# Kernel optimization log

Hardware: AMD Instinct MI355X
Metric: run time of the kernel (lower is better)

## Reference

```python
import jax, jax.numpy as jnp
import numpy as np

N_SRC, N_DST, K = 50000, 10000, 32
IN_F, OUT_F, H, L = 256, 128, 8, 10


def setup_inputs() -> dict:
    key = jax.random.key(0)
    ks = jax.random.split(key, 12)
    s = 0.05
    return {
        "feat": jax.random.normal(ks[0], (N_SRC, IN_F), jnp.float32),
        "labels": jax.random.uniform(ks[1], (N_SRC, L), jnp.float32),
        "labels_ori": jax.random.uniform(ks[2], (N_SRC, L), jnp.float32),
        "label_rela": jax.random.uniform(ks[3], (L, L), jnp.float32),
        "W_neigh": jax.random.normal(ks[4], (IN_F, OUT_F), jnp.float32) * s,
        "b_neigh": jnp.zeros((OUT_F,), jnp.float32),
        "W_self": jax.random.normal(ks[5], (IN_F, OUT_F), jnp.float32) * s,
        "b_self": jnp.zeros((OUT_F,), jnp.float32),
        "W_attn": jax.random.normal(ks[6], (2 * OUT_F, OUT_F * H), jnp.float32) * s,
        "b_attn": jnp.zeros((OUT_F * H,), jnp.float32),
        "feat_attn_W": jax.random.normal(ks[7], (1, H, OUT_F), jnp.float32) * s,
        "eps": jnp.full((1,), 0.5, jnp.float32),
        "out_bias": jnp.zeros((OUT_F,), jnp.float32),
        "nbr_idx": jax.random.randint(ks[8], (N_DST, K), 0, N_SRC, jnp.int32),
    }


def reference(feat, labels, labels_ori, label_rela, W_neigh, b_neigh, W_self,
              b_self, W_attn, b_attn, feat_attn_W, eps, out_bias, nbr_idx):
    n_dst = nbr_idx.shape[0]
    # lin_before_mp is True (in_feats > out_feats): fc_neigh applied to src feats
    h_src = feat @ W_neigh + b_neigh                      # (N_SRC, OUT_F)
    feat_dst = feat[:n_dst]
    cent_l = labels[:n_dst]                                # dst predicted labels
    cent_f = h_src[:n_dst]                                 # dst 'f' field
    # mailbox gather: fixed-fanout neighbors
    h = h_src[nbr_idx]                                     # (N, K, OUT_F)
    l_pred = labels[nbr_idx]                               # (N, K, L)
    # label similarity: sum(outer(l_pred_j, cent_l_i) * R)
    label_sim = jnp.einsum('nka,ab,nb->nk', l_pred, label_rela, cent_l)
    # feature attention score
    h_act = jax.nn.leaky_relu(h, negative_slope=0.1)
    cent_rep = jnp.broadcast_to(cent_f[:, None, :], h_act.shape)
    x = jnp.concatenate([h_act, cent_rep], axis=-1)        # (N, K, 2*OUT_F)
    t = (x @ W_attn + b_attn).reshape(n_dst, K, H, OUT_F)
    feat_sim = jnp.einsum('nkhd,hd->nk', t, feat_attn_W[0])
    # merge (torch.tensor(...) in the original detaches this from the graph)
    merge = jax.lax.stop_gradient(label_sim * eps[0] + feat_sim * (1.0 - eps[0]))
    att = jax.nn.softmax(merge, axis=1)                    # (N, K)
    neigh = (h * att[:, :, None]).mean(axis=1)             # (N, OUT_F)
    rst = (feat_dst @ W_self + b_self + neigh) * 0.5 + out_bias
    return rst, cent_l, labels_ori[:n_dst]
```

## Files before the change

kernel.cpp:

```cpp
#include <hip/hip_runtime.h>
#include <hip/hip_bf16.h>

#define N_SRC 50000
#define N_DST 10000
#define KNBR  32
#define IN_F  256
#define OUT_F 128
#define LDIM  10
#define ATTN_OUT 1024
#define NB_BIG  782
#define NB_SELF 157

using f32x4 = __attribute__((ext_vector_type(4))) float;
using s16x8 = __attribute__((ext_vector_type(8))) short;

#define OUT_CENT (N_DST*OUT_F)
#define OUT_LORI (N_DST*OUT_F + N_DST*LDIM)

#define WS_WCOMB 0
#define WS_BN    128
#define WS_BS    (128 + 16384)
#define WS_HSRC  (128 + 32768)
#define WS_SELF0 (128 + 32768 + (N_SRC*OUT_F/2))

__device__ __forceinline__ ushort f2bf(float x) {
  __hip_bfloat16 h = __float2bfloat16(x);
  return *reinterpret_cast<ushort*>(&h);
}

__global__ __launch_bounds__(256) void prep_kernel(
    const float* __restrict__ W_attn, const float* __restrict__ fW,
    const float* __restrict__ W_neigh, const float* __restrict__ W_self,
    float* __restrict__ w_comb, ushort* __restrict__ Bn, ushort* __restrict__ Bs) {
  const int b = blockIdx.x;
  const int t = threadIdx.x;
  if (b < 128) {
    __shared__ float red[256];
    float s = 0.f;
#pragma unroll
    for (int i = 0; i < 4; ++i) {
      int o = t + i * 256;
      s += W_attn[(size_t)b * ATTN_OUT + o] * fW[o];
    }
    red[t] = s;
    __syncthreads();
    for (int st = 128; st > 0; st >>= 1) {
      if (t < st) red[t] += red[t + st];
      __syncthreads();
    }
    if (t == 0) w_comb[b] = red[0];
  } else if (b < 256) {
    int k = 2 * (b - 128) + (t >> 7);
    int n = t & 127;
    float x = W_neigh[(size_t)k * OUT_F + n];
    Bn[(k >> 3) * 1024 + n * 8 + (k & 7)] = f2bf(x);
  } else {
    int k = 2 * (b - 256) + (t >> 7);
    int n = t & 127;
    float x = W_self[(size_t)k * OUT_F + n];
    Bs[(k >> 3) * 1024 + n * 8 + (k & 7)] = f2bf(x);
  }
}

template<bool OUT_BF16>
__device__ __forceinline__ void gemm_body(
    const float* __restrict__ A, const ushort* __restrict__ Bp,
    const float* __restrict__ bias, void* __restrict__ C, int M, int m0) {
  const int t = threadIdx.x;
  const int wv = t >> 6, ln = t & 63;
  const int dg = ln & 15, kg = ln >> 4;
  int r = m0 + wv * 16 + dg;
  r = r < M ? r : M - 1;

  f32x4 araw[16];
  const float* arow = &A[(size_t)r * IN_F];
#pragma unroll
  for (int k0 = 0; k0 < 8; ++k0) {
    const f32x4* ap = (const f32x4*)&arow[k0 * 32 + kg * 8];
    araw[2 * k0]     = ap[0];
    araw[2 * k0 + 1] = ap[1];
  }
  s16x8 afr[8];
#pragma unroll
  for (int k0 = 0; k0 < 8; ++k0) {
    s16x8 f;
    f[0] = (short)f2bf(araw[2*k0][0]); f[1] = (short)f2bf(araw[2*k0][1]);
    f[2] = (short)f2bf(araw[2*k0][2]); f[3] = (short)f2bf(araw[2*k0][3]);
    f[4] = (short)f2bf(araw[2*k0+1][0]); f[5] = (short)f2bf(araw[2*k0+1][1]);
    f[6] = (short)f2bf(araw[2*k0+1][2]); f[7] = (short)f2bf(araw[2*k0+1][3]);
    afr[k0] = f;
  }

  f32x4 acc[8];
#pragma unroll
  for (int ct = 0; ct < 8; ++ct) acc[ct] = (f32x4){0.f, 0.f, 0.f, 0.f};
#pragma unroll
  for (int k0 = 0; k0 < 8; ++k0) {
    const ushort* bb = Bp + (k0 * 4 + kg) * 1024 + dg * 8;
#pragma unroll
    for (int ct = 0; ct < 8; ++ct) {
      s16x8 bfr = *reinterpret_cast<const s16x8*>(bb + ct * 128);
      acc[ct] = __builtin_amdgcn_mfma_f32_16x16x32_bf16(afr[k0], bfr, acc[ct], 0, 0, 0);
    }
  }

#pragma unroll
  for (int ct = 0; ct < 8; ++ct) {
    int col = ct * 16 + dg;
    float bb = bias[col];
#pragma unroll
    for (int e = 0; e < 4; ++e) {
      int rr = m0 + wv * 16 + kg * 4 + e;
      if (rr < M) {
        float v = acc[ct][e] + bb;
        if (OUT_BF16) ((ushort*)C)[(size_t)rr * OUT_F + col] = f2bf(v);
        else          ((float*)C)[(size_t)rr * OUT_F + col] = v;
      }
    }
  }
}

__global__ __launch_bounds__(256) void fused_gemm(
    const float* __restrict__ A,
    const ushort* __restrict__ Bn, const ushort* __restrict__ Bs,
    const float* __restrict__ bias_n, const float* __restrict__ bias_s,
    ushort* __restrict__ hsrc, float* __restrict__ self0) {
  if (blockIdx.x < NB_BIG)
    gemm_body<true>(A, Bn, bias_n, (void*)hsrc, N_SRC, blockIdx.x * 64);
  else
    gemm_body<false>(A, Bs, bias_s, (void*)self0, N_DST, (blockIdx.x - NB_BIG) * 64);
}

__global__ __launch_bounds__(256) void attn_kernel(
    const float* __restrict__ labels, const float* __restrict__ labels_ori,
    const float* __restrict__ label_rela, const int* __restrict__ nbr_idx,
    const ushort* __restrict__ hsrc, const float* __restrict__ self0,
    const float* __restrict__ w_comb, const float* __restrict__ eps_p,
    const float* __restrict__ out_bias, float* __restrict__ out) {
  const int t = threadIdx.x;
  const int wv = t >> 6, ln = t & 63;
  const int n = blockIdx.x * 4 + wv;
  const int dg = ln & 15, kg = ln >> 4;

  const float eps = eps_p[0];
  const float om = 1.f - eps;

  float wcs[8];
  {
    const f32x4* wp = (const f32x4*)&w_comb[dg * 8];
    f32x4 w0 = wp[0], w1 = wp[1];
    wcs[0] = om * w0[0]; wcs[1] = om * w0[1]; wcs[2] = om * w0[2]; wcs[3] = om * w0[3];
    wcs[4] = om * w1[0]; wcs[5] = om * w1[1]; wcs[6] = om * w1[2]; wcs[7] = om * w1[3];
  }
  float va = 0.f;
  if (dg < LDIM) {
#pragma unroll
    for (int b = 0; b < LDIM; ++b)
      va += label_rela[dg * LDIM + b] * labels[(size_t)n * LDIM + b];
    va *= eps;
  }

  const int* irow = nbr_idx + (size_t)n * KNBR;
  float hf[8][8];
  float m[8];
#pragma unroll
  for (int j = 0; j < 8; ++j) {
    int id = irow[kg * 8 + j];
    uint4 hv = *(const uint4*)(hsrc + (size_t)id * OUT_F + dg * 8);
    hf[j][0] = __uint_as_float(hv.x << 16);
    hf[j][1] = __uint_as_float(hv.x & 0xffff0000u);
    hf[j][2] = __uint_as_float(hv.y << 16);
    hf[j][3] = __uint_as_float(hv.y & 0xffff0000u);
    hf[j][4] = __uint_as_float(hv.z << 16);
    hf[j][5] = __uint_as_float(hv.z & 0xffff0000u);
    hf[j][6] = __uint_as_float(hv.w << 16);
    hf[j][7] = __uint_as_float(hv.w & 0xffff0000u);
    float p = 0.f;
#pragma unroll
    for (int e = 0; e < 8; ++e)
      p = fmaf(fmaxf(hf[j][e], 0.1f * hf[j][e]), wcs[e], p);
    if (dg < LDIM) p = fmaf(labels[(size_t)id * LDIM + dg], va, p);
    m[j] = p;
  }
#pragma unroll
  for (int s = 1; s < 16; s <<= 1) {
#pragma unroll
    for (int j = 0; j < 8; ++j) m[j] += __shfl_xor(m[j], s);
  }
  float mx = m[0];
#pragma unroll
  for (int j = 1; j < 8; ++j) mx = fmaxf(mx, m[j]);
  mx = fmaxf(mx, __shfl_xor(mx, 16));
  mx = fmaxf(mx, __shfl_xor(mx, 32));
  float ssum = 0.f;
#pragma unroll
  for (int j = 0; j < 8; ++j) {
    m[j] = __expf(m[j] - mx);
    ssum += m[j];
  }
  ssum += __shfl_xor(ssum, 16);
  ssum += __shfl_xor(ssum, 32);
  const float scale = 1.f / (ssum * (float)KNBR);
  float pn[8];
#pragma unroll
  for (int e = 0; e < 8; ++e) pn[e] = 0.f;
#pragma unroll
  for (int j = 0; j < 8; ++j) {
#pragma unroll
    for (int e = 0; e < 8; ++e) pn[e] = fmaf(m[j], hf[j][e], pn[e]);
  }
#pragma unroll
  for (int e = 0; e < 8; ++e) {
    pn[e] += __shfl_xor(pn[e], 16);
    pn[e] += __shfl_xor(pn[e], 32);
  }
  if (kg == 0) {
    const float* srow = self0 + (size_t)n * OUT_F + dg * 8;
    float* orow = out + (size_t)n * OUT_F + dg * 8;
    f32x4 o0, o1;
#pragma unroll
    for (int e = 0; e < 4; ++e)
      o0[e] = (srow[e] + pn[e] * scale) * 0.5f + out_bias[dg * 8 + e];
#pragma unroll
    for (int e = 0; e < 4; ++e)
      o1[e] = (srow[4 + e] + pn[4 + e] * scale) * 0.5f + out_bias[dg * 8 + 4 + e];
    *(f32x4*)orow = o0;
    *(f32x4*)(orow + 4) = o1;
  }
  if (kg == 1 && dg < LDIM)
    out[OUT_CENT + (size_t)n * LDIM + dg] = labels[(size_t)n * LDIM + dg];
  if (kg == 2 && dg < LDIM)
    out[OUT_LORI + (size_t)n * LDIM + dg] = labels_ori[(size_t)n * LDIM + dg];
}

extern "C" void kernel_launch(void* const* d_in, const int* in_sizes, int n_in,
                              void* d_out, int out_size, void* d_ws, size_t ws_size,
                              hipStream_t stream) {
  const float* feat       = (const float*)d_in[0];
  const float* labels     = (const float*)d_in[1];
  const float* labels_ori = (const float*)d_in[2];
  const float* label_rela = (const float*)d_in[3];
  const float* W_neigh    = (const float*)d_in[4];
  const float* b_neigh    = (const float*)d_in[5];
  const float* W_self     = (const float*)d_in[6];
  const float* b_self     = (const float*)d_in[7];
  const float* W_attn     = (const float*)d_in[8];
  const float* fW         = (const float*)d_in[10];
  const float* eps        = (const float*)d_in[11];
  const float* out_bias   = (const float*)d_in[12];
  const int*   nbr_idx    = (const int*)d_in[13];

  float* wsf = (float*)d_ws;
  float* out = (float*)d_out;

  float*  w_comb = wsf + WS_WCOMB;
  ushort* Bn     = (ushort*)(wsf + WS_BN);
  ushort* Bsf    = (ushort*)(wsf + WS_BS);
  ushort* h_src  = (ushort*)(wsf + WS_HSRC);
  float*  self0  = wsf + WS_SELF0;

  prep_kernel<<<384, 256, 0, stream>>>(W_attn, fW, W_neigh, W_self, w_comb, Bn, Bsf);
  fused_gemm<<<NB_BIG + NB_SELF, 256, 0, stream>>>(feat, Bn, Bsf, b_neigh, b_self, h_src, self0);
  attn_kernel<<<(N_DST / 4), 256, 0, stream>>>(labels, labels_ori, label_rela, nbr_idx,
                                               h_src, self0, w_comb, eps, out_bias, out);
}
```

Before: 65.75 us.

## Precompute per-source feature attention score in GEMM epilogue, gather scalar in attn

The feature-similarity score leaky_relu(h)·w_comb depends only on the source node, so it is now computed once per source row in the GEMM epilogue from the fp32 accumulator and stored in a score array. The attention kernel gathers one scalar per neighbor instead of recomputing the dot product for each of the 32 neighbor occurrences. This removes redundant ALU work there. It also issues all neighbor row loads before use and adds launch_bounds occupancy hints. The cost is a cross-lane reduction in the GEMM epilogue and an extra small gather. The score now uses unrounded fp32 values rather than bf16-rounded ones, which slightly changes numerics.

```diff
diff --git a/kernel.cpp b/kernel.cpp
--- a/kernel.cpp
+++ b/kernel.cpp
@@ -22,6 +22,7 @@
 #define WS_BS    (128 + 16384)
 #define WS_HSRC  (128 + 32768)
 #define WS_SELF0 (128 + 32768 + (N_SRC*OUT_F/2))
+#define WS_SCORE (WS_SELF0 + N_DST*OUT_F)
 
 __device__ __forceinline__ ushort f2bf(float x) {
   __hip_bfloat16 h = __float2bfloat16(x);
@@ -65,30 +66,34 @@
 template<bool OUT_BF16>
 __device__ __forceinline__ void gemm_body(
     const float* __restrict__ A, const ushort* __restrict__ Bp,
-    const float* __restrict__ bias, void* __restrict__ C, int M, int m0) {
+    const float* __restrict__ bias, const float* __restrict__ w_comb,
+    void* __restrict__ C, float* __restrict__ score_f, int M, int m0) {
   const int t = threadIdx.x;
   const int wv = t >> 6, ln = t & 63;
   const int dg = ln & 15, kg = ln >> 4;
   int r = m0 + wv * 16 + dg;
   r = r < M ? r : M - 1;
-
-  f32x4 araw[16];
   const float* arow = &A[(size_t)r * IN_F];
-#pragma unroll
-  for (int k0 = 0; k0 < 8; ++k0) {
-    const f32x4* ap = (const f32x4*)&arow[k0 * 32 + kg * 8];
-    araw[2 * k0]     = ap[0];
-    araw[2 * k0 + 1] = ap[1];
-  }
+
   s16x8 afr[8];
 #pragma unroll
-  for (int k0 = 0; k0 < 8; ++k0) {
-    s16x8 f;
-    f[0] = (short)f2bf(araw[2*k0][0]); f[1] = (short)f2bf(araw[2*k0][1]);
-    f[2] = (short)f2bf(araw[2*k0][2]); f[3] = (short)f2bf(araw[2*k0][3]);
-    f[4] = (short)f2bf(araw[2*k0+1][0]); f[5] = (short)f2bf(araw[2*k0+1][1]);
-    f[6] = (short)f2bf(araw[2*k0+1][2]); f[7] = (short)f2bf(araw[2*k0+1][3]);
-    afr[k0] = f;
+  for (int half = 0; half < 2; ++half) {
+    f32x4 araw[8];
+#pragma unroll
+    for (int k0 = 0; k0 < 4; ++k0) {
+      const f32x4* ap = (const f32x4*)&arow[(half * 4 + k0) * 32 + kg * 8];
+      araw[2 * k0]     = ap[0];
+      araw[2 * k0 + 1] = ap[1];
+    }
+#pragma unroll
+    for (int k0 = 0; k0 < 4; ++k0) {
+      s16x8 f;
+      f[0] = (short)f2bf(araw[2*k0][0]); f[1] = (short)f2bf(araw[2*k0][1]);
+      f[2] = (short)f2bf(araw[2*k0][2]); f[3] = (short)f2bf(araw[2*k0][3]);
+      f[4] = (short)f2bf(araw[2*k0+1][0]); f[5] = (short)f2bf(araw[2*k0+1][1]);
+      f[6] = (short)f2bf(araw[2*k0+1][2]); f[7] = (short)f2bf(araw[2*k0+1][3]);
+      afr[half * 4 + k0] = f;
+    }
   }
 
   f32x4 acc[8];
@@ -104,38 +109,57 @@
     }
   }
 
+  float sc[4] = {0.f, 0.f, 0.f, 0.f};
 #pragma unroll
   for (int ct = 0; ct < 8; ++ct) {
     int col = ct * 16 + dg;
     float bb = bias[col];
+    float wc = OUT_BF16 ? w_comb[col] : 0.f;
 #pragma unroll
     for (int e = 0; e < 4; ++e) {
       int rr = m0 + wv * 16 + kg * 4 + e;
-      if (rr < M) {
-        float v = acc[ct][e] + bb;
-        if (OUT_BF16) ((ushort*)C)[(size_t)rr * OUT_F + col] = f2bf(v);
-        else          ((float*)C)[(size_t)rr * OUT_F + col] = v;
+      float v = acc[ct][e] + bb;
+      if (OUT_BF16) {
+        sc[e] = fmaf(fmaxf(v, 0.1f * v), wc, sc[e]);
+        if (rr < M) ((ushort*)C)[(size_t)rr * OUT_F + col] = f2bf(v);
+      } else {
+        if (rr < M) ((float*)C)[(size_t)rr * OUT_F + col] = v;
       }
     }
   }
-}
-
-__global__ __launch_bounds__(256) void fused_gemm(
+  if (OUT_BF16) {
+#pragma unroll
+    for (int s = 1; s < 16; s <<= 1) {
+#pragma unroll
+      for (int e = 0; e < 4; ++e) sc[e] += __shfl_xor(sc[e], s);
+    }
+    if (dg == 0) {
+#pragma unroll
+      for (int e = 0; e < 4; ++e) {
+        int rr = m0 + wv * 16 + kg * 4 + e;
+        if (rr < M) score_f[rr] = sc[e];
+      }
+    }
+  }
+}
+
+__global__ __launch_bounds__(256, 4) void fused_gemm(
     const float* __restrict__ A,
     const ushort* __restrict__ Bn, const ushort* __restrict__ Bs,
     const float* __restrict__ bias_n, const float* __restrict__ bias_s,
-    ushort* __restrict__ hsrc, float* __restrict__ self0) {
+    const float* __restrict__ w_comb,
+    ushort* __restrict__ hsrc, float* __restrict__ self0, float* __restrict__ score_f) {
   if (blockIdx.x < NB_BIG)
-    gemm_body<true>(A, Bn, bias_n, (void*)hsrc, N_SRC, blockIdx.x * 64);
+    gemm_body<true>(A, Bn, bias_n, w_comb, (void*)hsrc, score_f, N_SRC, blockIdx.x * 64);
   else
-    gemm_body<false>(A, Bs, bias_s, (void*)self0, N_DST, (blockIdx.x - NB_BIG) * 64);
-}
-
-__global__ __launch_bounds__(256) void attn_kernel(
+    gemm_body<false>(A, Bs, bias_s, w_comb, (void*)self0, score_f, N_DST, (blockIdx.x - NB_BIG) * 64);
+}
+
+__global__ __launch_bounds__(256, 4) void attn_kernel(
     const float* __restrict__ labels, const float* __restrict__ labels_ori,
     const float* __restrict__ label_rela, const int* __restrict__ nbr_idx,
     const ushort* __restrict__ hsrc, const float* __restrict__ self0,
-    const float* __restrict__ w_comb, const float* __restrict__ eps_p,
+    const float* __restrict__ score_f, const float* __restrict__ eps_p,
     const float* __restrict__ out_bias, float* __restrict__ out) {
   const int t = threadIdx.x;
   const int wv = t >> 6, ln = t & 63;
@@ -145,13 +169,6 @@
   const float eps = eps_p[0];
   const float om = 1.f - eps;
 
-  float wcs[8];
-  {
-    const f32x4* wp = (const f32x4*)&w_comb[dg * 8];
-    f32x4 w0 = wp[0], w1 = wp[1];
-    wcs[0] = om * w0[0]; wcs[1] = om * w0[1]; wcs[2] = om * w0[2]; wcs[3] = om * w0[3];
-    wcs[4] = om * w1[0]; wcs[5] = om * w1[1]; wcs[6] = om * w1[2]; wcs[7] = om * w1[3];
-  }
   float va = 0.f;
   if (dg < LDIM) {
 #pragma unroll
@@ -161,26 +178,20 @@
   }
 
   const int* irow = nbr_idx + (size_t)n * KNBR;
-  float hf[8][8];
+  int ids[8];
+  uint4 hv[8];
+#pragma unroll
+  for (int j = 0; j < 8; ++j) {
+    ids[j] = irow[kg * 8 + j];
+    hv[j] = *(const uint4*)(hsrc + (size_t)ids[j] * OUT_F + dg * 8);
+  }
   float m[8];
 #pragma unroll
   for (int j = 0; j < 8; ++j) {
-    int id = irow[kg * 8 + j];
-    uint4 hv = *(const uint4*)(hsrc + (size_t)id * OUT_F + dg * 8);
-    hf[j][0] = __uint_as_float(hv.x << 16);
-    hf[j][1] = __uint_as_float(hv.x & 0xffff0000u);
-    hf[j][2] = __uint_as_float(hv.y << 16);
-    hf[j][3] = __uint_as_float(hv.y & 0xffff0000u);
-    hf[j][4] = __uint_as_float(hv.z << 16);
-    hf[j][5] = __uint_as_float(hv.z & 0xffff0000u);
-    hf[j][6] = __uint_as_float(hv.w << 16);
-    hf[j][7] = __uint_as_float(hv.w & 0xffff0000u);
-    float p = 0.f;
-#pragma unroll
-    for (int e = 0; e < 8; ++e)
-      p = fmaf(fmaxf(hf[j][e], 0.1f * hf[j][e]), wcs[e], p);
-    if (dg < LDIM) p = fmaf(labels[(size_t)id * LDIM + dg], va, p);
-    m[j] = p;
+    float sp = 0.f;
+    if (dg == 0) sp = om * score_f[ids[j]];
+    if (dg < LDIM) sp = fmaf(labels[(size_t)ids[j] * LDIM + dg], va, sp);
+    m[j] = sp;
   }
 #pragma unroll
   for (int s = 1; s < 16; s <<= 1) {
@@ -206,8 +217,15 @@
   for (int e = 0; e < 8; ++e) pn[e] = 0.f;
 #pragma unroll
   for (int j = 0; j < 8; ++j) {
-#pragma unroll
-    for (int e = 0; e < 8; ++e) pn[e] = fmaf(m[j], hf[j][e], pn[e]);
+    float a = m[j];
+    pn[0] = fmaf(a, __uint_as_float(hv[j].x << 16), pn[0]);
+    pn[1] = fmaf(a, __uint_as_float(hv[j].x & 0xffff0000u), pn[1]);
+    pn[2] = fmaf(a, __uint_as_float(hv[j].y << 16), pn[2]);
+    pn[3] = fmaf(a, __uint_as_float(hv[j].y & 0xffff0000u), pn[3]);
+    pn[4] = fmaf(a, __uint_as_float(hv[j].z << 16), pn[4]);
+    pn[5] = fmaf(a, __uint_as_float(hv[j].z & 0xffff0000u), pn[5]);
+    pn[6] = fmaf(a, __uint_as_float(hv[j].w << 16), pn[6]);
+    pn[7] = fmaf(a, __uint_as_float(hv[j].w & 0xffff0000u), pn[7]);
   }
 #pragma unroll
   for (int e = 0; e < 8; ++e) {
@@ -253,14 +271,16 @@
   float* wsf = (float*)d_ws;
   float* out = (float*)d_out;
 
-  float*  w_comb = wsf + WS_WCOMB;
-  ushort* Bn     = (ushort*)(wsf + WS_BN);
-  ushort* Bsf    = (ushort*)(wsf + WS_BS);
-  ushort* h_src  = (ushort*)(wsf + WS_HSRC);
-  float*  self0  = wsf + WS_SELF0;
+  float*  w_comb  = wsf + WS_WCOMB;
+  ushort* Bn      = (ushort*)(wsf + WS_BN);
+  ushort* Bsf     = (ushort*)(wsf + WS_BS);
+  ushort* h_src   = (ushort*)(wsf + WS_HSRC);
+  float*  self0   = wsf + WS_SELF0;
+  float*  score_f = wsf + WS_SCORE;
 
   prep_kernel<<<384, 256, 0, stream>>>(W_attn, fW, W_neigh, W_self, w_comb, Bn, Bsf);
-  fused_gemm<<<NB_BIG + NB_SELF, 256, 0, stream>>>(feat, Bn, Bsf, b_neigh, b_self, h_src, self0);
+  fused_gemm<<<NB_BIG + NB_SELF, 256, 0, stream>>>(feat, Bn, Bsf, b_neigh, b_self,
+                                                   w_comb, h_src, self0, score_f);
   attn_kernel<<<(N_DST / 4), 256, 0, stream>>>(labels, labels_ori, label_rela, nbr_idx,
-                                               h_src, self0, w_comb, eps, out_bias, out);
-}
+                                               h_src, self0, score_f, eps, out_bias, out);
+}
```

New measurement: 59.63 us. 9.3% less time.
